# Kernel tuning notes

Hardware: AMD Instinct MI355X
Metric: run time of the kernel (lower is better)

The kernel has to match this reference:

```python
import jax, jax.numpy as jnp
import numpy as np

N_G, E_G, E_LG = 32768, 131072, 262144
H, NODE_DIM, EDGE_DIM, NB, EB = 128, 32, 16, 4, 4
L, B, TASKS = 4, 256, 10
EPS_MSG = 1e-7   # GENConv message epsilon
BN_EPS = 1e-5    # eval-mode batchnorm (running_mean=0, running_var=1)


def setup_inputs() -> dict:
    key = jax.random.key(0)
    ks = jax.random.split(key, 24)
    s = 0.05
    inp = {
        'x_g': jax.random.normal(ks[0], (N_G, NODE_DIM), jnp.float32),
        'edge_attr_g': jax.random.normal(ks[1], (E_G, EDGE_DIM), jnp.float32),
        'x_lg': jax.random.normal(ks[2], (E_G, NB), jnp.float32),
        'edge_dist_basis': jax.random.normal(ks[3], (E_G, NB), jnp.float32),
        'edge_attr_lg': jax.random.normal(ks[4], (E_LG, EB), jnp.float32),
        'edge_index_g': jax.random.randint(ks[5], (2, E_G), 0, N_G, jnp.int32),
        'edge_index_lg': jax.random.randint(ks[6], (2, E_LG), 0, E_G, jnp.int32),
        'batch_idx': jnp.sort(jax.random.randint(ks[7], (N_G,), 0, B, jnp.int32)),
        # parameters
        'W_enc': jax.random.normal(ks[8], (NODE_DIM, H), jnp.float32) * s,
        'b_enc': jnp.zeros((H,), jnp.float32),
        'W_msg': jax.random.normal(ks[9], (2 * H + EDGE_DIM + NB, H), jnp.float32) * s,
        'b_msg': jnp.zeros((H,), jnp.float32),
        'W_nb': jax.random.normal(ks[10], (NB, H), jnp.float32) * s,
        'b_nb': jnp.zeros((H,), jnp.float32),
        'W_eb': jax.random.normal(ks[11], (EB, H), jnp.float32) * s,
        'b_eb': jnp.zeros((H,), jnp.float32),
        'W_gcn': jax.random.normal(ks[12], (L, H, H), jnp.float32) * s,
        'b_gcn': jnp.zeros((L, H), jnp.float32),
        't_vals': jnp.ones((L,), jnp.float32),
        'gamma': jnp.ones((L, H), jnp.float32) + 0.1 * jax.random.normal(ks[13], (L, H), jnp.float32),
        'beta': 0.1 * jax.random.normal(ks[14], (L, H), jnp.float32),
        'W_pred': jax.random.normal(ks[15], (H, TASKS), jnp.float32) * s,
        'b_pred': jnp.zeros((TASKS,), jnp.float32),
    }
    return inp


def _forward(x_g, edge_attr_g, x_lg, edge_dist_basis, edge_attr_lg,
             W_enc, b_enc, W_msg, b_msg, W_nb, b_nb, W_eb, b_eb,
             W_gcn, b_gcn, t_vals, gamma, beta, W_pred, b_pred,
             edge_index_g, edge_index_lg, batch_idx):
    # node encode + build initial per-edge (line-graph node) message embedding
    h_node = x_g @ W_enc + b_enc                              # [N_g, H]
    src_g, dst_g = edge_index_g[0], edge_index_g[1]
    msg_cat = jnp.concatenate(
        [h_node[src_g], h_node[dst_g], edge_attr_g, x_lg], axis=-1)
    h = msg_cat @ W_msg + b_msg                               # [E_g, H]

    nb = edge_dist_basis @ W_nb + b_nb                        # [E_g, H] dist basis emb
    eb = edge_attr_lg @ W_eb + b_eb                           # [E_lg, H] angle basis emb
    src, dst = edge_index_lg[0], edge_index_lg[1]
    n_lg = h.shape[0]

    def genconv(x, W, b, t):
        # message: source msg gated by dist basis of source edge and angle basis
        m = jax.nn.relu(x[src] * nb[src] * eb) + EPS_MSG       # [E_lg, H]
        s = m * t
        mx = jax.ops.segment_max(s, dst, num_segments=n_lg)
        ex = jnp.exp(s - mx[dst])
        den = jax.ops.segment_sum(ex, dst, num_segments=n_lg)
        num = jax.ops.segment_sum(ex * m, dst, num_segments=n_lg)
        agg = num / jnp.where(den > 0, den, 1.0)               # softmax aggregation
        return (x + agg) @ W + b                               # 1-layer MLP update

    inv = 1.0 / jnp.sqrt(jnp.float32(1.0 + BN_EPS))

    def bn(x, g, bt):  # eval-mode BN with running stats (0, 1)
        return x * (inv * g) + bt

    h = genconv(h, W_gcn[0], b_gcn[0], t_vals[0])
    for l in range(1, L):  # res+ blocks (dropout off in eval)
        h2 = jax.nn.relu(bn(h, gamma[l - 1], beta[l - 1]))
        h = genconv(h2, W_gcn[l], b_gcn[l], t_vals[l]) + h
    h = bn(h, gamma[L - 1], beta[L - 1])

    node_emb = jax.ops.segment_sum(h, dst_g, num_segments=N_G)  # scatter_add back
    counts = jax.ops.segment_sum(jnp.ones((N_G,), h.dtype), batch_idx, num_segments=B)
    gsum = jax.ops.segment_sum(node_emb, batch_idx, num_segments=B)
    h_graph = gsum / jnp.maximum(counts, 1.0)[:, None]           # mean pool
    return h_graph @ W_pred + b_pred


def reference(x_g, edge_attr_g, x_lg, edge_dist_basis, edge_attr_lg,
              W_enc, b_enc, W_msg, b_msg, W_nb, b_nb, W_eb, b_eb,
              W_gcn, b_gcn, t_vals, gamma, beta, W_pred, b_pred,
              edge_index_g, edge_index_lg, batch_idx):
    return _forward(x_g, edge_attr_g, x_lg, edge_dist_basis, edge_attr_lg,
                    W_enc, b_enc, W_msg, b_msg, W_nb, b_nb, W_eb, b_eb,
                    W_gcn, b_gcn, t_vals, gamma, beta, W_pred, b_pred,
                    edge_index_g, edge_index_lg, batch_idx)
```

## Files before the change

### kernel.cpp

```cpp
#include <hip/hip_runtime.h>

typedef unsigned short u16;
typedef __attribute__((ext_vector_type(4))) float f32x4;
typedef __attribute__((ext_vector_type(8))) short short8;

#define N_G_   32768
#define E_G_   131072
#define E_LG_  262144
#define H_     128
#define B_     256
#define TASKS_ 10
#define KPAD_  288
#define LDST_  296
#define CPAD_  132
#define APAD_  136
#define SCAP_  256
#define INVBN_ 0.9999950000374997f
#define NCVT_  20
#define TOTAL_CANON_ 5352216

__device__ __forceinline__ float bf2f(u16 h){
  union { unsigned int u; float f; } v; v.u = ((unsigned int)h) << 16; return v.f;
}
__device__ __forceinline__ u16 f2bf(float f){
  union { float f; unsigned int u; } v; v.f = f;
  unsigned int u = v.u + 0x7fffu + ((v.u >> 16) & 1u);
  return (u16)(u >> 16);
}

__global__ void k_detect(const unsigned int* __restrict__ x, int* __restrict__ flag){
  __shared__ int sm[256];
  unsigned int v = x[threadIdx.x];
  unsigned int e = (v >> 7) & 0xFFu;
  sm[threadIdx.x] = (e >= 110u && e <= 140u) ? 1 : 0;
  __syncthreads();
  for (int s=128;s>0;s>>=1){ if (threadIdx.x < s) sm[threadIdx.x] += sm[threadIdx.x+s]; __syncthreads(); }
  if (threadIdx.x == 0) flag[0] = (sm[0] > 128) ? 1 : 0;
}

struct CvtArgs { const void* src[NCVT_]; int start[NCVT_]; int count[NCVT_]; };

__global__ void k_cvt(CvtArgs a, int total, const int* __restrict__ flag, u16* __restrict__ dst){
  int i = blockIdx.x*256 + threadIdx.x;
  if (i >= total) return;
  int s = 0;
  #pragma unroll
  for (int j=1;j<NCVT_;j++) if (i >= a.start[j]) s = j;
  int off = i - a.start[s];
  if (off >= a.count[s]) { dst[i] = 0; return; }
  if (flag[0]) dst[i] = ((const u16*)a.src[s])[off];
  else         dst[i] = f2bf(((const float*)a.src[s])[off]);
}

__global__ void k_pack(const u16* __restrict__ Wg, const u16* __restrict__ Wm,
                       u16* __restrict__ WTg, u16* __restrict__ WTm){
  int idx = blockIdx.x*256 + threadIdx.x;
  if (idx < 4*128*128){
    int l = idx >> 14, n = (idx >> 7) & 127, k = idx & 127;
    WTg[idx] = Wg[((l<<7) + k)*128 + n];
  }
  if (idx < 128*KPAD_){
    int n = idx / KPAD_, kp = idx % KPAD_;
    WTm[idx] = (kp < 276) ? Wm[kp*128 + n] : (u16)0;
  }
}

__global__ __launch_bounds__(256) void k_enc(const u16* __restrict__ xg, const u16* __restrict__ We,
                      const u16* __restrict__ be, u16* __restrict__ hn){
  int idx = blockIdx.x*256 + threadIdx.x;
  int r = idx >> 7, c = idx & 127;
  float acc = bf2f(be[c]);
  const u16* xr = xg + r*32;
  #pragma unroll
  for (int k=0;k<32;k++) acc += bf2f(xr[k]) * bf2f(We[k*128 + c]);
  hn[idx] = f2bf(acc);
}

__global__ __launch_bounds__(256) void k_msg(const u16* __restrict__ hn, const u16* __restrict__ eag,
     const u16* __restrict__ xlg, const int* __restrict__ eig,
     const u16* __restrict__ WTm, const u16* __restrict__ bmsg, u16* __restrict__ h){
  __shared__ __align__(16) u16 As[64*LDST_];
  int tid = threadIdx.x;
  int e0 = blockIdx.x * 64;
  {
    int i = tid >> 2;
    int j = tid & 3;
    int e = e0 + i;
    int s = eig[e];
    int d = eig[E_G_ + e];
    u16* rowp = As + i*LDST_;
    const u16* ps = hn + s*128 + j*32;
    const u16* pd = hn + d*128 + j*32;
    #pragma unroll
    for (int q=0;q<4;q++) *(short8*)(rowp + j*32 + q*8)       = *(const short8*)(ps + q*8);
    #pragma unroll
    for (int q=0;q<4;q++) *(short8*)(rowp + 128 + j*32 + q*8) = *(const short8*)(pd + q*8);
    if (j == 0){
      *(short8*)(rowp + 256) = *(const short8*)(eag + e*16);
      *(short8*)(rowp + 264) = *(const short8*)(eag + e*16 + 8);
      *(ushort4*)(rowp + 272) = *(const ushort4*)(xlg + e*4);
      *(ushort4*)(rowp + 276) = (ushort4){0,0,0,0};
      *(short8*)(rowp + 280) = (short8){0,0,0,0,0,0,0,0};
    }
  }
  __syncthreads();
  int wave = tid >> 6, lane = tid & 63, quad = lane >> 4, l16 = lane & 15;
  int arow = wave*16 + l16;
  f32x4 acc[8];
  #pragma unroll
  for (int ct=0;ct<8;ct++) acc[ct] = (f32x4){0.f,0.f,0.f,0.f};
  for (int ks=0; ks<KPAD_; ks+=32){
    short8 af = *(const short8*)(As + arow*LDST_ + ks + quad*8);
    #pragma unroll
    for (int ct=0;ct<8;ct++){
      short8 bfr = *(const short8*)(WTm + (ct*16 + l16)*KPAD_ + ks + quad*8);
      acc[ct] = __builtin_amdgcn_mfma_f32_16x16x32_bf16(af, bfr, acc[ct], 0,0,0);
    }
  }
  __syncthreads();
  float* Cs = (float*)As;
  {
    int lrow = wave*16 + quad*4;
    #pragma unroll
    for (int ct=0;ct<8;ct++){
      int col = ct*16 + l16;
      #pragma unroll
      for (int i=0;i<4;i++) Cs[(lrow+i)*CPAD_ + col] = acc[ct][i];
    }
  }
  __syncthreads();
  #pragma unroll
  for (int p=0;p<4;p++){
    int s = p*256 + tid;
    int lrow = s >> 4, c0 = (s & 15) * 8;
    const float* cp = Cs + lrow*CPAD_ + c0;
    short8 bs = *(const short8*)(bmsg + c0);
    short8 ov;
    #pragma unroll
    for (int k=0;k<8;k++) ov[k] = (short)f2bf(cp[k] + bf2f((u16)bs[k]));
    *(short8*)(h + (size_t)(e0 + lrow)*128 + c0) = ov;
  }
}

__global__ __launch_bounds__(256) void k_agg_gemm(
    const u16* __restrict__ gin,
    const u16* __restrict__ hres,
    const int* __restrict__ srcs, const int* __restrict__ off,
    const u16* __restrict__ w, const u16* __restrict__ tvals, int layer,
    const u16* __restrict__ WT, const u16* __restrict__ bg,
    const u16* __restrict__ gamma, const u16* __restrict__ beta,
    u16* __restrict__ hout, u16* __restrict__ h2out, int residual, int write_h2){
  __shared__ __align__(16) float Cs[16*CPAD_];
  __shared__ int srcs_s[SCAP_];
  u16* As = (u16*)Cs;
  int tid = threadIdx.x;
  int e0 = blockIdx.x*16;

  int kbB = off[e0], keB = off[e0+16];
  int cnt = keB - kbB;
  for (int i = tid; i < cnt && i < SCAP_; i += 256) srcs_s[i] = srcs[kbB + i];
  __syncthreads();

  {
    int r = tid >> 4;
    int c0 = (tid & 15) * 8;
    int g = e0 + r;
    float t = bf2f(tvals[layer]);
    float den[8]={0.f,0.f,0.f,0.f,0.f,0.f,0.f,0.f};
    float num[8]={0.f,0.f,0.f,0.f,0.f,0.f,0.f,0.f};
    int kb = off[g], ke = off[g+1];
    short8 xu, wu;
    if (kb < ke){
      int i0 = kb - kbB;
      int s0 = (i0 < SCAP_) ? srcs_s[i0] : srcs[kb];
      xu = *(const short8*)(gin + (size_t)s0*128 + c0);
      wu = *(const short8*)(w + (size_t)kb*128 + c0);
    }
    for (int k = kb; k < ke; k++){
      short8 xn, wn;
      if (k+1 < ke){
        int i1 = k+1 - kbB;
        int s1 = (i1 < SCAP_) ? srcs_s[i1] : srcs[k+1];
        xn = *(const short8*)(gin + (size_t)s1*128 + c0);
        wn = *(const short8*)(w + (size_t)(k+1)*128 + c0);
      }
      #pragma unroll
      for (int j=0;j<8;j++){
        float m  = fmaxf(bf2f((u16)xu[j])*bf2f((u16)wu[j]), 0.f);
        float e1 = __expf(m*t);
        den[j] += e1;
        num[j] = fmaf(e1, m, num[j]);
      }
      xu = xn; wu = wn;
    }
    short8 xdu = *(const short8*)(gin + (size_t)g*128 + c0);
    short8 ov;
    #pragma unroll
    for (int j=0;j<8;j++)
      ov[j] = (short)f2bf(bf2f((u16)xdu[j]) + (den[j] > 0.f ? num[j]/den[j] : 0.f));
    *(short8*)(As + r*APAD_ + c0) = ov;
  }
  __syncthreads();

  int wave = tid >> 6, lane = tid & 63, quad = lane >> 4, l16 = lane & 15;
  f32x4 acc[2];
  acc[0] = (f32x4){0.f,0.f,0.f,0.f};
  acc[1] = (f32x4){0.f,0.f,0.f,0.f};
  #pragma unroll
  for (int ks=0;ks<128;ks+=32){
    short8 af = *(const short8*)(As + l16*APAD_ + ks + quad*8);
    #pragma unroll
    for (int c2=0;c2<2;c2++){
      int ct = wave*2 + c2;
      short8 bfr = *(const short8*)(WT + (ct*16 + l16)*128 + ks + quad*8);
      acc[c2] = __builtin_amdgcn_mfma_f32_16x16x32_bf16(af, bfr, acc[c2], 0,0,0);
    }
  }
  __syncthreads();
  {
    int lrow = quad*4;
    #pragma unroll
    for (int c2=0;c2<2;c2++){
      int col = (wave*2 + c2)*16 + l16;
      #pragma unroll
      for (int i=0;i<4;i++) Cs[(lrow+i)*CPAD_ + col] = acc[c2][i];
    }
  }
  __syncthreads();

  {
    int lrow = tid >> 4, ce = (tid & 15) * 8;
    const float* cp = Cs + lrow*CPAD_ + ce;
    size_t goff = (size_t)(e0 + lrow)*128 + ce;
    short8 bs = *(const short8*)(bg + ce);
    float v[8];
    #pragma unroll
    for (int k=0;k<8;k++) v[k] = cp[k] + bf2f((u16)bs[k]);
    if (residual){
      short8 hs = *(const short8*)(hres + goff);
      #pragma unroll
      for (int k=0;k<8;k++) v[k] += bf2f((u16)hs[k]);
    }
    short8 ov;
    #pragma unroll
    for (int k=0;k<8;k++) ov[k] = (short)f2bf(v[k]);
    *(short8*)(hout + goff) = ov;
    if (write_h2){
      short8 gs = *(const short8*)(gamma + layer*128 + ce);
      short8 es = *(const short8*)(beta  + layer*128 + ce);
      short8 o2;
      #pragma unroll
      for (int k=0;k<8;k++)
        o2[k] = (short)f2bf(fmaxf(fmaf(v[k], bf2f((u16)gs[k])*INVBN_, bf2f((u16)es[k])), 0.f));
      *(short8*)(h2out + goff) = o2;
    }
  }
}

__global__ void k_count_both(const int* __restrict__ eilg_dst, const int* __restrict__ eig_dst,
                             int* __restrict__ cnt1, int* __restrict__ cnt2){
  int i = blockIdx.x*256 + threadIdx.x;
  if (i < E_LG_) atomicAdd(&cnt1[eilg_dst[i]], 1);
  else {
    int j = i - E_LG_;
    if (j < E_G_) atomicAdd(&cnt2[eig_dst[j]], 1);
  }
}
__global__ void k_bsum_both(const int* __restrict__ cnt1, const int* __restrict__ cnt2,
                            int* __restrict__ bsum){
  __shared__ int sm[256];
  int b = blockIdx.x;
  int v;
  if (b < 512) v = cnt1[b*256 + threadIdx.x];
  else         v = cnt2[(b-512)*256 + threadIdx.x];
  sm[threadIdx.x] = v;
  __syncthreads();
  for (int s=128;s>0;s>>=1){ if (threadIdx.x < s) sm[threadIdx.x] += sm[threadIdx.x+s]; __syncthreads(); }
  if (threadIdx.x==0) bsum[b] = sm[0];
}
__global__ void k_scanb_both(const int* __restrict__ bsum, int* __restrict__ bbase,
                             int* __restrict__ off1, int* __restrict__ off2){
  __shared__ int sm[1024];
  int t = threadIdx.x;
  {
    int v = (t < 512) ? bsum[t] : 0;
    sm[t] = v; __syncthreads();
    for (int d=1; d<1024; d<<=1){
      int u = (t>=d) ? sm[t-d] : 0;
      __syncthreads();
      sm[t] += u;
      __syncthreads();
    }
    if (t < 512) bbase[t] = sm[t] - v;
    if (t == 511) off1[E_G_] = sm[511];
  }
  __syncthreads();
  {
    int v = (t < 128) ? bsum[512 + t] : 0;
    sm[t] = v; __syncthreads();
    for (int d=1; d<1024; d<<=1){
      int u = (t>=d) ? sm[t-d] : 0;
      __syncthreads();
      sm[t] += u;
      __syncthreads();
    }
    if (t < 128) bbase[512 + t] = sm[t] - v;
    if (t == 127) off2[N_G_] = sm[127];
  }
}
__global__ void k_offsets_both(int* __restrict__ cnt1, int* __restrict__ cnt2,
                               const int* __restrict__ bbase,
                               int* __restrict__ off1, int* __restrict__ off2){
  __shared__ int sm[256];
  int b = blockIdx.x;
  int t = threadIdx.x;
  int* cnt; int* off; int i;
  if (b < 512){ cnt = cnt1; off = off1; i = b*256 + t; }
  else        { cnt = cnt2; off = off2; i = (b-512)*256 + t; }
  int v = cnt[i];
  cnt[i] = 0;
  sm[t] = v; __syncthreads();
  for (int d=1; d<256; d<<=1){
    int u = (t>=d) ? sm[t-d] : 0;
    __syncthreads();
    sm[t] += u;
    __syncthreads();
  }
  off[i] = bbase[b] + sm[t] - v;
}
__global__ void k_scatter_both(const int* __restrict__ eilg, const int* __restrict__ eig,
                               const int* __restrict__ off1, int* __restrict__ cnt1,
                               const int* __restrict__ off2, int* __restrict__ cnt2,
                               int* __restrict__ srcs, int* __restrict__ eidp,
                               int* __restrict__ eids){
  int i = blockIdx.x*256 + threadIdx.x;
  if (i < E_LG_){
    int s = eilg[i], d = eilg[E_LG_ + i];
    int p = off1[d] + atomicAdd(&cnt1[d], 1);
    srcs[p] = s;
    eidp[p] = i;
  } else {
    int e = i - E_LG_;
    if (e < E_G_){
      int d = eig[E_G_ + e];
      int p = off2[d] + atomicAdd(&cnt2[d], 1);
      eids[p] = e;
    }
  }
}

__global__ __launch_bounds__(256) void k_wprep(const int* __restrict__ srcs, const int* __restrict__ eidp,
    const u16* __restrict__ dbas, const u16* __restrict__ ealg,
    const u16* __restrict__ Wnb, const u16* __restrict__ bnb,
    const u16* __restrict__ Web, const u16* __restrict__ beb,
    u16* __restrict__ w){
  int c0 = (threadIdx.x & 15) * 8;
  float wnb[4][8], web[4][8], vbn[8], vbe[8];
  #pragma unroll
  for (int i=0;i<4;i++){
    short8 a = *(const short8*)(Wnb + i*128 + c0);
    short8 b = *(const short8*)(Web + i*128 + c0);
    #pragma unroll
    for (int j=0;j<8;j++){ wnb[i][j]=bf2f((u16)a[j]); web[i][j]=bf2f((u16)b[j]); }
  }
  {
    short8 a = *(const short8*)(bnb + c0);
    short8 b = *(const short8*)(beb + c0);
    #pragma unroll
    for (int j=0;j<8;j++){ vbn[j]=bf2f((u16)a[j]); vbe[j]=bf2f((u16)b[j]); }
  }
  int g0 = blockIdx.x*16 + (threadIdx.x >> 4);
  int gs = gridDim.x*16;
  for (int p = g0; p < E_LG_; p += gs){
    int sidx = srcs[p];
    int eidx = eidp[p];
    ushort4 du = *(const ushort4*)(dbas + sidx*4);
    ushort4 eu = *(const ushort4*)(ealg + eidx*4);
    float db[4] = {bf2f(du.x), bf2f(du.y), bf2f(du.z), bf2f(du.w)};
    float ev[4] = {bf2f(eu.x), bf2f(eu.y), bf2f(eu.z), bf2f(eu.w)};
    short8 ov;
    #pragma unroll
    for (int j=0;j<8;j++){
      float nbv = vbn[j] + db[0]*wnb[0][j] + db[1]*wnb[1][j] + db[2]*wnb[2][j] + db[3]*wnb[3][j];
      float ebv = vbe[j] + ev[0]*web[0][j] + ev[1]*web[1][j] + ev[2]*web[2][j] + ev[3]*web[3][j];
      ov[j] = (short)f2bf(nbv * ebv);
    }
    *(short8*)(w + (size_t)p*128 + c0) = ov;
  }
}

__global__ __launch_bounds__(256) void k_pool_nodes(const u16* __restrict__ h, const int* __restrict__ off2,
    const int* __restrict__ eids,
    const u16* __restrict__ gamma, const u16* __restrict__ beta,
    float* __restrict__ node_emb){
  int tid = blockIdx.x*256 + threadIdx.x;
  int n = tid >> 5;
  int c0 = (tid & 31)*4;
  ushort4 ga = *(const ushort4*)(gamma + 3*128 + c0);
  ushort4 be = *(const ushort4*)(beta + 3*128 + c0);
  float gg[4] = {bf2f(ga.x)*INVBN_, bf2f(ga.y)*INVBN_, bf2f(ga.z)*INVBN_, bf2f(ga.w)*INVBN_};
  float bt[4] = {bf2f(be.x), bf2f(be.y), bf2f(be.z), bf2f(be.w)};
  float s[4] = {0.f,0.f,0.f,0.f};
  int kb = off2[n], ke = off2[n+1];
  for (int k=kb; k<ke; k++){
    int e = eids[k];
    ushort4 xu = *(const ushort4*)(h + (size_t)e*128 + c0);
    float xs[4] = {bf2f(xu.x), bf2f(xu.y), bf2f(xu.z), bf2f(xu.w)};
    #pragma unroll
    for (int j=0;j<4;j++) s[j] += fmaf(xs[j], gg[j], bt[j]);
  }
  f32x4 ov = {s[0], s[1], s[2], s[3]};
  *(f32x4*)(node_emb + (size_t)n*128 + c0) = ov;
}

__global__ __launch_bounds__(128) void k_poolpred(const float* __restrict__ node_emb,
    const int* __restrict__ bidx,
    const u16* __restrict__ Wp, const u16* __restrict__ bp,
    const int* __restrict__ flag, void* __restrict__ out){
  int b = blockIdx.x;
  int t = threadIdx.x;
  int lo = 0, hi_s = N_G_;
  { int l = 0, r = N_G_;
    while (l < r){ int m = (l+r)>>1; if (bidx[m] < b) l = m+1; else r = m; }
    lo = l;
    l = lo; r = N_G_;
    while (l < r){ int m = (l+r)>>1; if (bidx[m] < b+1) l = m+1; else r = m; }
    hi_s = l;
  }
  float s = 0.f;
  for (int n=lo; n<hi_s; n++) s += node_emb[(size_t)n*128 + t];
  __shared__ float sm[128];
  sm[t] = s;
  __syncthreads();
  if (t < TASKS_){
    float inv = 1.0f / fmaxf((float)(hi_s - lo), 1.0f);
    float acc = bf2f(bp[t]);
    #pragma unroll 4
    for (int c=0;c<128;c++) acc += sm[c]*inv * bf2f(Wp[c*TASKS_ + t]);
    if (flag[0]) ((u16*)out)[b*TASKS_ + t] = f2bf(acc);
    else         ((float*)out)[b*TASKS_ + t] = acc;
  }
}

extern "C" void kernel_launch(void* const* d_in, const int* in_sizes, int n_in,
                              void* d_out, int out_size, void* d_ws, size_t ws_size,
                              hipStream_t stream){
  const int* eig  = (const int*)d_in[5];
  const int* eilg = (const int*)d_in[6];
  const int* bidx = (const int*)d_in[7];

  char* ws = (char*)d_ws; size_t o = 0;
  auto carve = [&](size_t b)->char*{ char* p = ws + o; o += (b + 255) & ~(size_t)255; return p; };
  int*  flag  = (int*) carve(256);
  u16*  canon = (u16*) carve((size_t)TOTAL_CANON_*2);
  u16*  hr0   = (u16*) carve((size_t)E_G_*H_*2);
  u16*  hr1   = (u16*) carve((size_t)E_G_*H_*2);
  u16*  ht0   = (u16*) carve((size_t)E_G_*H_*2);
  u16*  ht1   = (u16*) carve((size_t)E_G_*H_*2);
  u16*  hn    = (u16*) carve((size_t)N_G_*H_*2);
  u16*  WTg   = (u16*) carve((size_t)4*128*128*2);
  u16*  WTm   = (u16*) carve((size_t)128*KPAD_*2);
  int*  cntB  = (int*) carve((size_t)(E_G_+N_G_)*4);
  int*  cnt1  = cntB;
  int*  cnt2  = cntB + E_G_;
  int*  off1  = (int*) carve((size_t)(E_G_+1)*4);
  int*  off2  = (int*) carve((size_t)(N_G_+1)*4);
  int*  srcs  = (int*) carve((size_t)E_LG_*4);
  int*  eidp  = (int*) carve((size_t)E_LG_*4);
  int*  eids  = (int*) carve((size_t)E_G_*4);
  int*  bsum  = (int*) carve(1024*4);
  int*  bbase = (int*) carve(1024*4);
  float* node_emb = (float*)carve((size_t)N_G_*H_*4);
  u16* w_sorted = (u16*)carve((size_t)E_LG_*H_*2);
  (void)in_sizes; (void)n_in; (void)out_size; (void)ws_size;

  static const int di[NCVT_] = {0,1,2,3,4, 8,9,10,11,12,13,14,15,16,17,18,19,20,21,22};
  static const int st[NCVT_] = {0,1048576,3145728,3670016,4194304,
                                5242880,5246976,5247104,5282432,5282560,
                                5283072,5283200,5283712,5283840,5349376,
                                5349888,5349896,5350408,5350920,5352200};
  static const int cn[NCVT_] = {1048576,2097152,524288,524288,1048576,
                                4096,128,35328,128,512,
                                128,512,128,65536,512,
                                4,512,512,1280,10};
  CvtArgs ca;
  for (int i=0;i<NCVT_;i++){ ca.src[i]=d_in[di[i]]; ca.start[i]=st[i]; ca.count[i]=cn[i]; }

  const u16* x_g   = canon + st[0];
  const u16* ea_g  = canon + st[1];
  const u16* x_lg  = canon + st[2];
  const u16* dbas  = canon + st[3];
  const u16* ea_lg = canon + st[4];
  const u16* W_enc = canon + st[5];
  const u16* b_enc = canon + st[6];
  const u16* W_msg = canon + st[7];
  const u16* b_msg = canon + st[8];
  const u16* W_nb  = canon + st[9];
  const u16* b_nb  = canon + st[10];
  const u16* W_eb  = canon + st[11];
  const u16* b_eb  = canon + st[12];
  const u16* W_gcn = canon + st[13];
  const u16* b_gcn = canon + st[14];
  const u16* t_vals= canon + st[15];
  const u16* gamma = canon + st[16];
  const u16* beta  = canon + st[17];
  const u16* W_pred= canon + st[18];
  const u16* b_pred= canon + st[19];

  k_detect<<<1,256,0,stream>>>((const unsigned int*)d_in[0], flag);
  k_cvt<<<(TOTAL_CANON_+255)/256,256,0,stream>>>(ca, TOTAL_CANON_, flag, canon);

  k_pack<<<256,256,0,stream>>>(W_gcn, W_msg, WTg, WTm);
  k_enc<<<N_G_*H_/256,256,0,stream>>>(x_g, W_enc, b_enc, hn);
  k_msg<<<E_G_/64,256,0,stream>>>(hn, ea_g, x_lg, eig, WTm, b_msg, hr0);

  hipMemsetAsync(cntB, 0, (size_t)(E_G_+N_G_)*4, stream);
  k_count_both<<<(E_LG_+E_G_)/256,256,0,stream>>>(eilg + E_LG_, eig + E_G_, cnt1, cnt2);
  k_bsum_both<<<640,256,0,stream>>>(cnt1, cnt2, bsum);
  k_scanb_both<<<1,1024,0,stream>>>(bsum, bbase, off1, off2);
  k_offsets_both<<<640,256,0,stream>>>(cnt1, cnt2, bbase, off1, off2);
  k_scatter_both<<<(E_LG_+E_G_)/256,256,0,stream>>>(eilg, eig, off1, cnt1, off2, cnt2,
                                                    srcs, eidp, eids);

  k_wprep<<<2048,256,0,stream>>>(srcs, eidp, dbas, ea_lg, W_nb, b_nb, W_eb, b_eb, w_sorted);

  u16* hr[2] = {hr0, hr1};
  u16* ht[2] = {ht0, ht1};
  for (int l=0; l<4; l++){
    int pi = l & 1;
    int po = pi ^ 1;
    const u16* gin  = (l == 0) ? hr0 : ht[pi];
    const u16* hres = hr[pi];
    k_agg_gemm<<<E_G_/16,256,0,stream>>>(gin, hres, srcs, off1, w_sorted, t_vals, l,
        WTg + (size_t)l*128*128, b_gcn + l*128, gamma, beta,
        hr[po], ht[po], (l>0)?1:0, (l<3)?1:0);
  }

  k_pool_nodes<<<N_G_*32/256,256,0,stream>>>(hr[0], off2, eids, gamma, beta, node_emb);
  k_poolpred<<<B_,128,0,stream>>>(node_emb, bidx, W_pred, b_pred, flag, d_out);
}
```

Before: 561.7 us.

## Sort line-graph destinations by in-degree to balance aggregation work per block

```diff
diff --git a/kernel.cpp b/kernel.cpp
--- a/kernel.cpp
+++ b/kernel.cpp
@@ -14,7 +14,6 @@
 #define LDST_  296
 #define CPAD_  132
 #define APAD_  136
-#define SCAP_  256
 #define INVBN_ 0.9999950000374997f
 #define NCVT_  20
 #define TOTAL_CANON_ 5352216
@@ -146,41 +145,43 @@
     const u16* __restrict__ gin,
     const u16* __restrict__ hres,
     const int* __restrict__ srcs, const int* __restrict__ off,
+    const int* __restrict__ dperm,
     const u16* __restrict__ w, const u16* __restrict__ tvals, int layer,
     const u16* __restrict__ WT, const u16* __restrict__ bg,
     const u16* __restrict__ gamma, const u16* __restrict__ beta,
     u16* __restrict__ hout, u16* __restrict__ h2out, int residual, int write_h2){
   __shared__ __align__(16) float Cs[16*CPAD_];
-  __shared__ int srcs_s[SCAP_];
+  __shared__ int srcs_s[16][16];
+  __shared__ int dp_s[16];
   u16* As = (u16*)Cs;
   int tid = threadIdx.x;
   int e0 = blockIdx.x*16;
 
-  int kbB = off[e0], keB = off[e0+16];
-  int cnt = keB - kbB;
-  for (int i = tid; i < cnt && i < SCAP_; i += 256) srcs_s[i] = srcs[kbB + i];
+  if (tid < 16) dp_s[tid] = dperm[e0 + tid];
   __syncthreads();
 
   {
     int r = tid >> 4;
-    int c0 = (tid & 15) * 8;
-    int g = e0 + r;
+    int l16i = tid & 15;
+    int c0 = l16i * 8;
+    int g = dp_s[r];
+    int kb = off[g], ke = off[g+1];
+    int deg = ke - kb;
+    if (l16i < deg && l16i < 16) srcs_s[r][l16i] = srcs[kb + l16i];
     float t = bf2f(tvals[layer]);
     float den[8]={0.f,0.f,0.f,0.f,0.f,0.f,0.f,0.f};
     float num[8]={0.f,0.f,0.f,0.f,0.f,0.f,0.f,0.f};
-    int kb = off[g], ke = off[g+1];
     short8 xu, wu;
     if (kb < ke){
-      int i0 = kb - kbB;
-      int s0 = (i0 < SCAP_) ? srcs_s[i0] : srcs[kb];
+      int s0 = srcs_s[r][0];
       xu = *(const short8*)(gin + (size_t)s0*128 + c0);
       wu = *(const short8*)(w + (size_t)kb*128 + c0);
     }
     for (int k = kb; k < ke; k++){
       short8 xn, wn;
       if (k+1 < ke){
-        int i1 = k+1 - kbB;
-        int s1 = (i1 < SCAP_) ? srcs_s[i1] : srcs[k+1];
+        int i1 = k+1 - kb;
+        int s1 = (i1 < 16) ? srcs_s[r][i1] : srcs[k+1];
         xn = *(const short8*)(gin + (size_t)s1*128 + c0);
         wn = *(const short8*)(w + (size_t)(k+1)*128 + c0);
       }
@@ -230,8 +231,9 @@
 
   {
     int lrow = tid >> 4, ce = (tid & 15) * 8;
+    int g = dp_s[lrow];
     const float* cp = Cs + lrow*CPAD_ + ce;
-    size_t goff = (size_t)(e0 + lrow)*128 + ce;
+    size_t goff = (size_t)g*128 + ce;
     short8 bs = *(const short8*)(bg + ce);
     float v[8];
     #pragma unroll
@@ -347,6 +349,41 @@
       eids[p] = e;
     }
   }
+}
+
+__global__ void k_deghist(const int* __restrict__ off1, int* __restrict__ hist){
+  __shared__ int lh[33];
+  int t = threadIdx.x;
+  if (t < 33) lh[t] = 0;
+  __syncthreads();
+  int d = blockIdx.x*256 + t;
+  int deg = off1[d+1] - off1[d];
+  if (deg > 32) deg = 32;
+  atomicAdd(&lh[deg], 1);
+  __syncthreads();
+  if (t < 33 && lh[t] > 0) atomicAdd(&hist[t], lh[t]);
+}
+__global__ void k_degbase(const int* __restrict__ hist, int* __restrict__ cur){
+  if (threadIdx.x == 0){
+    int s = 0;
+    for (int i=0;i<33;i++){ cur[i] = s; s += hist[i]; }
+  }
+}
+__global__ void k_degscatter(const int* __restrict__ off1, int* __restrict__ cur,
+                             int* __restrict__ dperm){
+  __shared__ int lh[33];
+  __shared__ int bb[33];
+  int t = threadIdx.x;
+  if (t < 33) lh[t] = 0;
+  __syncthreads();
+  int d = blockIdx.x*256 + t;
+  int deg = off1[d+1] - off1[d];
+  if (deg > 32) deg = 32;
+  int lrank = atomicAdd(&lh[deg], 1);
+  __syncthreads();
+  if (t < 33 && lh[t] > 0) bb[t] = atomicAdd(&cur[t], lh[t]);
+  __syncthreads();
+  dperm[bb[deg] + lrank] = d;
 }
 
 __global__ __launch_bounds__(256) void k_wprep(const int* __restrict__ srcs, const int* __restrict__ eidp,
@@ -468,6 +505,9 @@
   int*  srcs  = (int*) carve((size_t)E_LG_*4);
   int*  eidp  = (int*) carve((size_t)E_LG_*4);
   int*  eids  = (int*) carve((size_t)E_G_*4);
+  int*  dperm = (int*) carve((size_t)E_G_*4);
+  int*  dhist = (int*) carve(64*4);
+  int*  dcur  = dhist + 33;
   int*  bsum  = (int*) carve(1024*4);
   int*  bbase = (int*) carve(1024*4);
   float* node_emb = (float*)carve((size_t)N_G_*H_*4);
@@ -515,6 +555,7 @@
   k_msg<<<E_G_/64,256,0,stream>>>(hn, ea_g, x_lg, eig, WTm, b_msg, hr0);
 
   hipMemsetAsync(cntB, 0, (size_t)(E_G_+N_G_)*4, stream);
+  hipMemsetAsync(dhist, 0, 64*4, stream);
   k_count_both<<<(E_LG_+E_G_)/256,256,0,stream>>>(eilg + E_LG_, eig + E_G_, cnt1, cnt2);
   k_bsum_both<<<640,256,0,stream>>>(cnt1, cnt2, bsum);
   k_scanb_both<<<1,1024,0,stream>>>(bsum, bbase, off1, off2);
@@ -522,6 +563,9 @@
   k_scatter_both<<<(E_LG_+E_G_)/256,256,0,stream>>>(eilg, eig, off1, cnt1, off2, cnt2,
                                                     srcs, eidp, eids);
 
+  k_deghist<<<E_G_/256,256,0,stream>>>(off1, dhist);
+  k_degbase<<<1,64,0,stream>>>(dhist, dcur);
+  k_degscatter<<<E_G_/256,256,0,stream>>>(off1, dcur, dperm);
   k_wprep<<<2048,256,0,stream>>>(srcs, eidp, dbas, ea_lg, W_nb, b_nb, W_eb, b_eb, w_sorted);
 
   u16* hr[2] = {hr0, hr1};
@@ -531,7 +575,7 @@
     int po = pi ^ 1;
     const u16* gin  = (l == 0) ? hr0 : ht[pi];
     const u16* hres = hr[pi];
-    k_agg_gemm<<<E_G_/16,256,0,stream>>>(gin, hres, srcs, off1, w_sorted, t_vals, l,
+    k_agg_gemm<<<E_G_/16,256,0,stream>>>(gin, hres, srcs, off1, dperm, w_sorted, t_vals, l,
         WTg + (size_t)l*128*128, b_gcn + l*128, gamma, beta,
         hr[po], ht[po], (l>0)?1:0, (l<3)?1:0);
   }
```

New measurement: 580.9 us. 3.4% more time.

## Fold node encoder into message weights and store node embeddings as bf16

Applied to the files above, without the earlier changes.

```diff
diff --git a/kernel.cpp b/kernel.cpp
--- a/kernel.cpp
+++ b/kernel.cpp
@@ -10,8 +10,8 @@
 #define H_     128
 #define B_     256
 #define TASKS_ 10
-#define KPAD_  288
-#define LDST_  296
+#define KC_    96
+#define LDSTC_ 104
 #define CPAD_  132
 #define APAD_  136
 #define SCAP_  256
@@ -53,54 +53,71 @@
 }
 
 __global__ void k_pack(const u16* __restrict__ Wg, const u16* __restrict__ Wm,
-                       u16* __restrict__ WTg, u16* __restrict__ WTm){
+                       const u16* __restrict__ Wenc, const u16* __restrict__ benc,
+                       const u16* __restrict__ bmsg,
+                       u16* __restrict__ WTg, u16* __restrict__ WTc, u16* __restrict__ bC){
   int idx = blockIdx.x*256 + threadIdx.x;
   if (idx < 4*128*128){
     int l = idx >> 14, n = (idx >> 7) & 127, k = idx & 127;
     WTg[idx] = Wg[((l<<7) + k)*128 + n];
-  }
-  if (idx < 128*KPAD_){
-    int n = idx / KPAD_, kp = idx % KPAD_;
-    WTm[idx] = (kp < 276) ? Wm[kp*128 + n] : (u16)0;
-  }
-}
-
-__global__ __launch_bounds__(256) void k_enc(const u16* __restrict__ xg, const u16* __restrict__ We,
-                      const u16* __restrict__ be, u16* __restrict__ hn){
-  int idx = blockIdx.x*256 + threadIdx.x;
-  int r = idx >> 7, c = idx & 127;
-  float acc = bf2f(be[c]);
-  const u16* xr = xg + r*32;
-  #pragma unroll
-  for (int k=0;k<32;k++) acc += bf2f(xr[k]) * bf2f(We[k*128 + c]);
-  hn[idx] = f2bf(acc);
-}
-
-__global__ __launch_bounds__(256) void k_msg(const u16* __restrict__ hn, const u16* __restrict__ eag,
+    return;
+  }
+  int i2 = idx - 4*128*128;
+  if (i2 < 128*KC_){
+    int n = i2 / KC_, k = i2 % KC_;
+    float v = 0.f;
+    if (k < 32){
+      for (int j=0;j<128;j++) v += bf2f(Wenc[k*128 + j]) * bf2f(Wm[j*128 + n]);
+    } else if (k < 64){
+      int kk = k - 32;
+      for (int j=0;j<128;j++) v += bf2f(Wenc[kk*128 + j]) * bf2f(Wm[(128+j)*128 + n]);
+    } else if (k < 80){
+      v = bf2f(Wm[(256 + k - 64)*128 + n]);
+    } else if (k < 84){
+      v = bf2f(Wm[(272 + k - 80)*128 + n]);
+    }
+    WTc[n*KC_ + k] = f2bf(v);
+    return;
+  }
+  int i3 = i2 - 128*KC_;
+  if (i3 < 128){
+    int n = i3;
+    float v = bf2f(bmsg[n]);
+    for (int j=0;j<128;j++)
+      v += bf2f(benc[j]) * (bf2f(Wm[j*128 + n]) + bf2f(Wm[(128+j)*128 + n]));
+    bC[n] = f2bf(v);
+  }
+}
+
+__global__ __launch_bounds__(256) void k_msg(const u16* __restrict__ xg, const u16* __restrict__ eag,
      const u16* __restrict__ xlg, const int* __restrict__ eig,
-     const u16* __restrict__ WTm, const u16* __restrict__ bmsg, u16* __restrict__ h){
-  __shared__ __align__(16) u16 As[64*LDST_];
+     const u16* __restrict__ WTc, const u16* __restrict__ bC, u16* __restrict__ h){
+  __shared__ __align__(16) float Cs[64*CPAD_];
+  u16* As = (u16*)Cs;
   int tid = threadIdx.x;
   int e0 = blockIdx.x * 64;
   {
     int i = tid >> 2;
     int j = tid & 3;
     int e = e0 + i;
-    int s = eig[e];
-    int d = eig[E_G_ + e];
-    u16* rowp = As + i*LDST_;
-    const u16* ps = hn + s*128 + j*32;
-    const u16* pd = hn + d*128 + j*32;
-    #pragma unroll
-    for (int q=0;q<4;q++) *(short8*)(rowp + j*32 + q*8)       = *(const short8*)(ps + q*8);
-    #pragma unroll
-    for (int q=0;q<4;q++) *(short8*)(rowp + 128 + j*32 + q*8) = *(const short8*)(pd + q*8);
+    u16* rowp = As + i*LDSTC_;
     if (j == 0){
-      *(short8*)(rowp + 256) = *(const short8*)(eag + e*16);
-      *(short8*)(rowp + 264) = *(const short8*)(eag + e*16 + 8);
-      *(ushort4*)(rowp + 272) = *(const ushort4*)(xlg + e*4);
-      *(ushort4*)(rowp + 276) = (ushort4){0,0,0,0};
-      *(short8*)(rowp + 280) = (short8){0,0,0,0,0,0,0,0};
+      int s = eig[e];
+      const u16* ps = xg + s*32;
+      #pragma unroll
+      for (int q=0;q<4;q++) *(short8*)(rowp + q*8) = *(const short8*)(ps + q*8);
+    } else if (j == 1){
+      int d = eig[E_G_ + e];
+      const u16* pd = xg + d*32;
+      #pragma unroll
+      for (int q=0;q<4;q++) *(short8*)(rowp + 32 + q*8) = *(const short8*)(pd + q*8);
+    } else if (j == 2){
+      *(short8*)(rowp + 64) = *(const short8*)(eag + e*16);
+      *(short8*)(rowp + 72) = *(const short8*)(eag + e*16 + 8);
+    } else {
+      *(ushort4*)(rowp + 80) = *(const ushort4*)(xlg + e*4);
+      *(ushort4*)(rowp + 84) = (ushort4){0,0,0,0};
+      *(short8*)(rowp + 88) = (short8){0,0,0,0,0,0,0,0};
     }
   }
   __syncthreads();
@@ -109,16 +126,16 @@
   f32x4 acc[8];
   #pragma unroll
   for (int ct=0;ct<8;ct++) acc[ct] = (f32x4){0.f,0.f,0.f,0.f};
-  for (int ks=0; ks<KPAD_; ks+=32){
-    short8 af = *(const short8*)(As + arow*LDST_ + ks + quad*8);
+  #pragma unroll
+  for (int ks=0; ks<KC_; ks+=32){
+    short8 af = *(const short8*)(As + arow*LDSTC_ + ks + quad*8);
     #pragma unroll
     for (int ct=0;ct<8;ct++){
-      short8 bfr = *(const short8*)(WTm + (ct*16 + l16)*KPAD_ + ks + quad*8);
+      short8 bfr = *(const short8*)(WTc + (ct*16 + l16)*KC_ + ks + quad*8);
       acc[ct] = __builtin_amdgcn_mfma_f32_16x16x32_bf16(af, bfr, acc[ct], 0,0,0);
     }
   }
   __syncthreads();
-  float* Cs = (float*)As;
   {
     int lrow = wave*16 + quad*4;
     #pragma unroll
@@ -134,7 +151,7 @@
     int s = p*256 + tid;
     int lrow = s >> 4, c0 = (s & 15) * 8;
     const float* cp = Cs + lrow*CPAD_ + c0;
-    short8 bs = *(const short8*)(bmsg + c0);
+    short8 bs = *(const short8*)(bC + c0);
     short8 ov;
     #pragma unroll
     for (int k=0;k<8;k++) ov[k] = (short)f2bf(cp[k] + bf2f((u16)bs[k]));
@@ -392,7 +409,7 @@
 __global__ __launch_bounds__(256) void k_pool_nodes(const u16* __restrict__ h, const int* __restrict__ off2,
     const int* __restrict__ eids,
     const u16* __restrict__ gamma, const u16* __restrict__ beta,
-    float* __restrict__ node_emb){
+    u16* __restrict__ node_emb){
   int tid = blockIdx.x*256 + threadIdx.x;
   int n = tid >> 5;
   int c0 = (tid & 31)*4;
@@ -409,11 +426,12 @@
     #pragma unroll
     for (int j=0;j<4;j++) s[j] += fmaf(xs[j], gg[j], bt[j]);
   }
-  f32x4 ov = {s[0], s[1], s[2], s[3]};
-  *(f32x4*)(node_emb + (size_t)n*128 + c0) = ov;
-}
-
-__global__ __launch_bounds__(128) void k_poolpred(const float* __restrict__ node_emb,
+  ushort4 ov;
+  ov.x = f2bf(s[0]); ov.y = f2bf(s[1]); ov.z = f2bf(s[2]); ov.w = f2bf(s[3]);
+  *(ushort4*)(node_emb + (size_t)n*128 + c0) = ov;
+}
+
+__global__ __launch_bounds__(128) void k_poolpred(const u16* __restrict__ node_emb,
     const int* __restrict__ bidx,
     const u16* __restrict__ Wp, const u16* __restrict__ bp,
     const int* __restrict__ flag, void* __restrict__ out){
@@ -428,7 +446,7 @@
     hi_s = l;
   }
   float s = 0.f;
-  for (int n=lo; n<hi_s; n++) s += node_emb[(size_t)n*128 + t];
+  for (int n=lo; n<hi_s; n++) s += bf2f(node_emb[(size_t)n*128 + t]);
   __shared__ float sm[128];
   sm[t] = s;
   __syncthreads();
@@ -457,9 +475,9 @@
   u16*  hr1   = (u16*) carve((size_t)E_G_*H_*2);
   u16*  ht0   = (u16*) carve((size_t)E_G_*H_*2);
   u16*  ht1   = (u16*) carve((size_t)E_G_*H_*2);
-  u16*  hn    = (u16*) carve((size_t)N_G_*H_*2);
   u16*  WTg   = (u16*) carve((size_t)4*128*128*2);
-  u16*  WTm   = (u16*) carve((size_t)128*KPAD_*2);
+  u16*  WTc   = (u16*) carve((size_t)128*KC_*2);
+  u16*  bC    = (u16*) carve((size_t)128*2);
   int*  cntB  = (int*) carve((size_t)(E_G_+N_G_)*4);
   int*  cnt1  = cntB;
   int*  cnt2  = cntB + E_G_;
@@ -470,8 +488,8 @@
   int*  eids  = (int*) carve((size_t)E_G_*4);
   int*  bsum  = (int*) carve(1024*4);
   int*  bbase = (int*) carve(1024*4);
-  float* node_emb = (float*)carve((size_t)N_G_*H_*4);
-  u16* w_sorted = (u16*)carve((size_t)E_LG_*H_*2);
+  u16*  node_emb = (u16*)carve((size_t)N_G_*H_*2);
+  u16*  w_sorted = (u16*)carve((size_t)E_LG_*H_*2);
   (void)in_sizes; (void)n_in; (void)out_size; (void)ws_size;
 
   static const int di[NCVT_] = {0,1,2,3,4, 8,9,10,11,12,13,14,15,16,17,18,19,20,21,22};
@@ -510,9 +528,9 @@
   k_detect<<<1,256,0,stream>>>((const unsigned int*)d_in[0], flag);
   k_cvt<<<(TOTAL_CANON_+255)/256,256,0,stream>>>(ca, TOTAL_CANON_, flag, canon);
 
-  k_pack<<<256,256,0,stream>>>(W_gcn, W_msg, WTg, WTm);
-  k_enc<<<N_G_*H_/256,256,0,stream>>>(x_g, W_enc, b_enc, hn);
-  k_msg<<<E_G_/64,256,0,stream>>>(hn, ea_g, x_lg, eig, WTm, b_msg, hr0);
+  k_pack<<<(4*128*128 + 128*KC_ + 128 + 255)/256,256,0,stream>>>(
+      W_gcn, W_msg, W_enc, b_enc, b_msg, WTg, WTc, bC);
+  k_msg<<<E_G_/64,256,0,stream>>>(x_g, ea_g, x_lg, eig, WTc, bC, hr0);
 
   hipMemsetAsync(cntB, 0, (size_t)(E_G_+N_G_)*4, stream);
   k_count_both<<<(E_LG_+E_G_)/256,256,0,stream>>>(eilg + E_LG_, eig + E_G_, cnt1, cnt2);
```

New measurement: 514.8 us. 8.3% less time.
